# Kernel tuning notes

Measured on AMD Instinct MI355X. Metric: run time of the kernel, lower is better.

## Reference

```python
import jax, jax.numpy as jnp
import numpy as np

MAX_LENGTH = 64
SOS_TOKEN = 0
B, S, H, V = 32, 64, 512, 32000


def setup_inputs() -> dict:
    key = jax.random.key(0)
    ks = jax.random.split(key, 12)
    w = 0.02  # weight init scale to keep tanh/sigmoid in sane range
    return {
        "encoder_outputs": jax.random.normal(ks[0], (B, S, H), jnp.float32),
        "encoder_hidden": jax.random.normal(ks[1], (1, B, H), jnp.float32),
        "target_tensor": jax.random.randint(ks[2], (B, MAX_LENGTH), 0, V),
        "emb": jax.random.normal(ks[3], (V, H), jnp.float32) * w,
        "Wa": jax.random.normal(ks[4], (H, H), jnp.float32) * w,
        "ba": jnp.zeros((H,), jnp.float32),
        "Ua": jax.random.normal(ks[5], (H, H), jnp.float32) * w,
        "bu": jnp.zeros((H,), jnp.float32),
        "Va": jax.random.normal(ks[6], (1, H), jnp.float32) * w,
        "bv": jnp.zeros((1,), jnp.float32),
        "W_ih": jax.random.normal(ks[7], (3 * H, 2 * H), jnp.float32) * w,
        "b_ih": jnp.zeros((3 * H,), jnp.float32),
        "W_hh": jax.random.normal(ks[8], (3 * H, H), jnp.float32) * w,
        "b_hh": jnp.zeros((3 * H,), jnp.float32),
        "Wout": jax.random.normal(ks[9], (V, H), jnp.float32) * w,
        "bout": jnp.zeros((V,), jnp.float32),
    }


def reference(encoder_outputs, encoder_hidden, target_tensor, emb, Wa, ba, Ua, bu,
              Va, bv, W_ih, b_ih, W_hh, b_hh, Wout, bout):
    # Teacher-forced decode: step 0 uses SOS, step i uses target[:, i-1].
    tokens = jnp.concatenate(
        [jnp.full((target_tensor.shape[0], 1), SOS_TOKEN, target_tensor.dtype),
         target_tensor[:, :-1]], axis=1)  # [B, T]
    keys_proj = jnp.einsum('bsh,gh->bsg', encoder_outputs, Ua) + bu  # Ua(keys), step-invariant
    h_dim = encoder_hidden.shape[-1]
    va = Va[0]

    def step(h, tok):  # h: [B,H], tok: [B]
        x = emb[tok]                                   # embedding (dropout = identity in eval)
        q = h @ Wa.T + ba                              # Wa(query)  [B,H]
        e = jnp.tanh(q[:, None, :] + keys_proj)        # [B,S,H]
        scores = jnp.einsum('bsh,h->bs', e, va) + bv[0]
        w = jax.nn.softmax(scores, axis=-1)            # [B,S]
        context = jnp.einsum('bs,bsh->bh', w, encoder_outputs)
        xin = jnp.concatenate([x, context], axis=-1)   # [B,2H]
        gi = xin @ W_ih.T + b_ih                       # [B,3H]
        gh = h @ W_hh.T + b_hh
        r = jax.nn.sigmoid(gi[:, :h_dim] + gh[:, :h_dim])
        z = jax.nn.sigmoid(gi[:, h_dim:2 * h_dim] + gh[:, h_dim:2 * h_dim])
        n = jnp.tanh(gi[:, 2 * h_dim:] + r * gh[:, 2 * h_dim:])
        h_new = (1.0 - z) * n + z * h
        logits = h_new @ Wout.T + bout                 # [B,V]
        return h_new, (logits, w)

    h0 = encoder_hidden[0]
    hT, (logits, attn) = jax.lax.scan(step, h0, tokens.T)  # logits [T,B,V], attn [T,B,S]
    decoder_outputs = jax.nn.log_softmax(jnp.transpose(logits, (1, 0, 2)), axis=-1)
    attentions = jnp.transpose(attn, (1, 0, 2))
    return decoder_outputs, hT[None], attentions


if __name__ == "__main__":
    out = reference(**setup_inputs())
    print([o.shape for o in out])
```

## Files before the change

### kernel.cpp

```cpp
#include <hip/hip_runtime.h>
#include <stdint.h>

typedef __bf16 bf16;
typedef __bf16 bf16x4 __attribute__((ext_vector_type(4)));
typedef __bf16 bf16x8 __attribute__((ext_vector_type(8)));
typedef float f32x4 __attribute__((ext_vector_type(4)));

#define NB_REC 256

__device__ __forceinline__ float fast_tanh(float x) {
  x = fminf(fmaxf(x, -15.f), 15.f);
  float u = __expf(2.f * x);
  return (u - 1.f) / (u + 1.f);
}
__device__ __forceinline__ float fast_sigmoid(float x) {
  return 1.f / (1.f + __expf(-x));
}

__global__ __launch_bounds__(256) void f2bf_k(const float* __restrict__ s,
                                              bf16* __restrict__ d, long n) {
  long i = ((long)blockIdx.x * 256 + threadIdx.x) * 4;
  if (i >= n) return;
  float4 v = *(const float4*)(s + i);
  bf16x4 o = {(bf16)v.x, (bf16)v.y, (bf16)v.z, (bf16)v.w};
  *(bf16x4*)(d + i) = o;
}

__global__ __launch_bounds__(256) void split_wih_k(const float* __restrict__ W,
                                                   bf16* __restrict__ X,
                                                   bf16* __restrict__ Cc) {
  long i = ((long)blockIdx.x * 256 + threadIdx.x) * 4;
  if (i >= (long)1536 * 512) return;
  long j = i >> 9, k = i & 511;
  float4 a = *(const float4*)(W + j * 1024 + k);
  float4 b = *(const float4*)(W + j * 1024 + 512 + k);
  bf16x4 oa = {(bf16)a.x, (bf16)a.y, (bf16)a.z, (bf16)a.w};
  bf16x4 ob = {(bf16)b.x, (bf16)b.y, (bf16)b.z, (bf16)b.w};
  *(bf16x4*)(X + i) = oa;
  *(bf16x4*)(Cc + i) = ob;
}

__global__ __launch_bounds__(256) void embed_k(const int* __restrict__ tgt,
                                               const float* __restrict__ emb,
                                               bf16* __restrict__ xe) {
  long i = ((long)blockIdx.x * 256 + threadIdx.x) * 4;
  if (i >= (long)2048 * 512) return;
  long m = i >> 9, k = i & 511;
  int b = (int)(m >> 6), t = (int)(m & 63);
  int tok = (t == 0) ? 0 : tgt[b * 64 + t - 1];
  float4 v = *(const float4*)(emb + (long)tok * 512 + k);
  bf16x4 o = {(bf16)v.x, (bf16)v.y, (bf16)v.z, (bf16)v.w};
  *(bf16x4*)(xe + i) = o;
}

__global__ __launch_bounds__(256) void kpt_k(const float* __restrict__ kp,
                                             float* __restrict__ kpT) {
  long i = (long)blockIdx.x * 256 + threadIdx.x;
  if (i >= (long)32 * 512 * 64) return;
  int b = (int)(i >> 15);
  int r = (int)(i & 32767);
  int k = r >> 6, s = r & 63;
  kpT[i] = kp[((long)b * 64 + s) * 512 + k];
}

__global__ __launch_bounds__(256) void gemm_bt(const bf16* __restrict__ A,
                                               const bf16* __restrict__ Bm,
                                               const float* __restrict__ bias,
                                               float* __restrict__ C, int N) {
  __shared__ bf16 As[128 * 32];
  __shared__ bf16 Bs[128 * 32];
  const int tid = threadIdx.x;
  const int bx = blockIdx.x;
  const int bm = bx & 15;
  const int bn = bx >> 4;
  const int lane = tid & 63;
  const int w = tid >> 6;
  const int l16 = lane & 15, q4 = lane >> 4;
  const int wm = (w & 1) * 64, wn = (w >> 1) * 64;
  const long m0 = (long)bm * 128;
  const long n0 = (long)bn * 128;
  const int r0 = tid >> 2;
  const int kp8 = (tid & 3) * 8;

  f32x4 acc[4][4] = {};
  for (int kk = 0; kk < 512; kk += 32) {
    __syncthreads();
    {
      bf16x8 va0 = *(const bf16x8*)(A + (m0 + r0) * 512 + kk + kp8);
      bf16x8 va1 = *(const bf16x8*)(A + (m0 + 64 + r0) * 512 + kk + kp8);
      bf16x8 vb0 = *(const bf16x8*)(Bm + (n0 + r0) * 512 + kk + kp8);
      bf16x8 vb1 = *(const bf16x8*)(Bm + (n0 + 64 + r0) * 512 + kk + kp8);
      *(bf16x8*)&As[r0 * 32 + kp8] = va0;
      *(bf16x8*)&As[(64 + r0) * 32 + kp8] = va1;
      *(bf16x8*)&Bs[r0 * 32 + kp8] = vb0;
      *(bf16x8*)&Bs[(64 + r0) * 32 + kp8] = vb1;
    }
    __syncthreads();
    bf16x8 af[4], bfr[4];
#pragma unroll
    for (int i = 0; i < 4; ++i)
      af[i] = *(const bf16x8*)&As[(wm + i * 16 + l16) * 32 + q4 * 8];
#pragma unroll
    for (int j = 0; j < 4; ++j)
      bfr[j] = *(const bf16x8*)&Bs[(wn + j * 16 + l16) * 32 + q4 * 8];
#pragma unroll
    for (int i = 0; i < 4; ++i)
#pragma unroll
      for (int j = 0; j < 4; ++j)
        acc[i][j] = __builtin_amdgcn_mfma_f32_16x16x32_bf16(af[i], bfr[j], acc[i][j], 0, 0, 0);
  }
#pragma unroll
  for (int i = 0; i < 4; ++i) {
    const long rbase = m0 + wm + i * 16 + q4 * 4;
#pragma unroll
    for (int j = 0; j < 4; ++j) {
      const long col = n0 + wn + j * 16 + l16;
      const float bv = bias ? bias[col] : 0.f;
      f32x4 a = acc[i][j];
      C[(rbase + 0) * N + col] = a[0] + bv;
      C[(rbase + 1) * N + col] = a[1] + bv;
      C[(rbase + 2) * N + col] = a[2] + bv;
      C[(rbase + 3) * N + col] = a[3] + bv;
    }
  }
}

__device__ __forceinline__ void gbar(unsigned* bar, int g, unsigned epoch) {
  __syncthreads();
  if (threadIdx.x == 0) {
    __builtin_amdgcn_s_waitcnt(0);
    __atomic_signal_fence(__ATOMIC_SEQ_CST);
    unsigned a = __hip_atomic_fetch_add(&bar[(g >> 5) * 16], 1u,
                                        __ATOMIC_RELAXED, __HIP_MEMORY_SCOPE_AGENT);
    if ((a & 31u) == 31u)
      __hip_atomic_fetch_add(&bar[128], 1u, __ATOMIC_RELAXED, __HIP_MEMORY_SCOPE_AGENT);
    while (__hip_atomic_load(&bar[128], __ATOMIC_RELAXED, __HIP_MEMORY_SCOPE_AGENT) <
           epoch * 8u)
      __builtin_amdgcn_s_sleep(2);
    __atomic_signal_fence(__ATOMIC_SEQ_CST);
  }
  __syncthreads();
}

__device__ __forceinline__ unsigned long long coh_load_u64(const unsigned long long* p) {
  return __hip_atomic_load(p, __ATOMIC_RELAXED, __HIP_MEMORY_SCOPE_AGENT);
}
__device__ __forceinline__ float coh_load_f32(const float* p) {
  return __hip_atomic_load(p, __ATOMIC_RELAXED, __HIP_MEMORY_SCOPE_AGENT);
}

__global__ __launch_bounds__(256) void recurrence_k(
    const bf16* __restrict__ Wc,
    const float* __restrict__ ba,
    const float* __restrict__ bhh,
    const float* __restrict__ ehid,
    unsigned long long* __restrict__ h_bfg,
    bf16* __restrict__ histb,
    float* __restrict__ QG,
    const float* __restrict__ kpT,
    const float* __restrict__ va,
    const float* __restrict__ gix,
    const float* __restrict__ ep,
    float* __restrict__ outhT,
    float* __restrict__ outattn,
    unsigned* __restrict__ bar) {
  const int g = blockIdx.x;
  const int tid = threadIdx.x;
  const int b = g & 31;
  const int p = g >> 5;
  __shared__ float va_s[512], q_s[512], part_s[256], w_s[64];
  __shared__ float gi_s[192], gh_s[192], h_loc[64];
  unsigned epoch = 0;

  va_s[tid] = va[tid];
  va_s[256 + tid] = va[256 + tid];
  if (tid < 64) h_loc[tid] = ehid[b * 512 + p * 64 + tid];
  if (g < 32 && tid < 128) {
    const float* hr = ehid + g * 512 + tid * 4;
    union { bf16 h[4]; unsigned long long u; } cv;
    cv.h[0] = (bf16)hr[0]; cv.h[1] = (bf16)hr[1];
    cv.h[2] = (bf16)hr[2]; cv.h[3] = (bf16)hr[3];
    __hip_atomic_store(&h_bfg[g * 128 + tid], cv.u, __ATOMIC_RELAXED,
                       __HIP_MEMORY_SCOPE_AGENT);
  }
  ++epoch;
  gbar(bar, g, epoch);

  for (int t = 0; t < 64; ++t) {
    if (g < 128 && tid < 64) {
      const int l16 = tid & 15, q4 = tid >> 4;
      const int n0 = g * 16;
      const bf16* bp = Wc + (long)(n0 + l16) * 512 + q4 * 8;
      const unsigned long long* a0p = h_bfg + l16 * 128 + q4 * 2;
      const unsigned long long* a1p = h_bfg + (16 + l16) * 128 + q4 * 2;
      f32x4 acc0 = {}, acc1 = {};
#pragma unroll
      for (int it = 0; it < 16; ++it) {
        union { unsigned long long u[2]; bf16x8 v; } A0, A1;
        A0.u[0] = coh_load_u64(a0p + it * 8 + 0);
        A0.u[1] = coh_load_u64(a0p + it * 8 + 1);
        A1.u[0] = coh_load_u64(a1p + it * 8 + 0);
        A1.u[1] = coh_load_u64(a1p + it * 8 + 1);
        bf16x8 bb = *(const bf16x8*)(bp + it * 32);
        acc0 = __builtin_amdgcn_mfma_f32_16x16x32_bf16(A0.v, bb, acc0, 0, 0, 0);
        acc1 = __builtin_amdgcn_mfma_f32_16x16x32_bf16(A1.v, bb, acc1, 0, 0, 0);
      }
      const int col = n0 + l16;
      const float badd = (col < 512) ? ba[col] : bhh[col - 512];
#pragma unroll
      for (int r = 0; r < 4; ++r) {
        __hip_atomic_store(&QG[(q4 * 4 + r) * 2048 + col], acc0[r] + badd,
                           __ATOMIC_RELAXED, __HIP_MEMORY_SCOPE_AGENT);
        __hip_atomic_store(&QG[(16 + q4 * 4 + r) * 2048 + col], acc1[r] + badd,
                           __ATOMIC_RELAXED, __HIP_MEMORY_SCOPE_AGENT);
      }
    }
    ++epoch;
    gbar(bar, g, epoch);

    q_s[tid] = coh_load_f32(&QG[b * 2048 + tid]);
    q_s[256 + tid] = coh_load_f32(&QG[b * 2048 + 256 + tid]);
    if (tid < 192) {
      const int part = tid >> 6, jj = tid & 63;
      gh_s[tid] = coh_load_f32(&QG[b * 2048 + 512 + part * 512 + p * 64 + jj]);
    }
    __syncthreads();

    {
      const int w = tid >> 6, l = tid & 63;
      const float* kprow = kpT + ((long)b * 512 + w * 128) * 64 + l;
      float acc = 0.f;
#pragma unroll 4
      for (int k = 0; k < 128; ++k)
        acc += va_s[w * 128 + k] * fast_tanh(q_s[w * 128 + k] + kprow[(long)k * 64]);
      part_s[w * 64 + l] = acc;
    }
    __syncthreads();
    if (tid < 64) {
      float sc = part_s[tid] + part_s[64 + tid] + part_s[128 + tid] + part_s[192 + tid];
      float e = __expf(sc);
      float sum = e;
#pragma unroll
      for (int d = 1; d < 64; d <<= 1) sum += __shfl_xor(sum, d);
      float wv = e / sum;
      w_s[tid] = wv;
      if (p == 0) outattn[(long)(b * 64 + t) * 64 + tid] = wv;
    }
    __syncthreads();

    if (tid < 192) {
      const int part = tid >> 6, jj = tid & 63;
      const int col = part * 512 + p * 64 + jj;
      const float* er = ep + (long)(b * 64) * 1536 + col;
      float acc = 0.f;
#pragma unroll 8
      for (int s2 = 0; s2 < 64; ++s2) acc += w_s[s2] * er[(long)s2 * 1536];
      gi_s[tid] = acc + gix[(long)(b * 64 + t) * 1536 + col];
    }
    __syncthreads();

    if (tid < 64) {
      float rr = fast_sigmoid(gi_s[tid] + gh_s[tid]);
      float zz = fast_sigmoid(gi_s[64 + tid] + gh_s[64 + tid]);
      float nn = fast_tanh(gi_s[128 + tid] + rr * gh_s[128 + tid]);
      float hp = h_loc[tid];
      float hn = (1.f - zz) * nn + zz * hp;
      h_loc[tid] = hn;
      const int j = p * 64 + tid;
      histb[(long)(b * 64 + t) * 512 + j] = (bf16)hn;
      if (t == 63) outhT[b * 512 + j] = hn;
      float hn1 = __shfl_xor(hn, 1);
      if ((tid & 1) == 0) {
        union { bf16 h[2]; unsigned u; } cv;
        cv.h[0] = (bf16)hn; cv.h[1] = (bf16)hn1;
        unsigned* h32v = (unsigned*)h_bfg;
        __hip_atomic_store(&h32v[b * 256 + (j >> 1)], cv.u, __ATOMIC_RELAXED,
                           __HIP_MEMORY_SCOPE_AGENT);
      }
    }
    ++epoch;
    gbar(bar, g, epoch);
  }
}

__global__ __launch_bounds__(256) void logsm_k(float* __restrict__ C) {
  const long row = blockIdx.x;
  float* x = C + row * 32000L;
  const int tid = threadIdx.x;
  __shared__ float red[4];
  float s = 0.f;
  for (long i = (long)tid * 4; i < 32000; i += 1024) {
    float4 v = *(const float4*)(x + i);
    s += __expf(v.x);
    s += __expf(v.y);
    s += __expf(v.z);
    s += __expf(v.w);
  }
#pragma unroll
  for (int d = 1; d < 64; d <<= 1) s += __shfl_xor(s, d);
  if ((tid & 63) == 0) red[tid >> 6] = s;
  __syncthreads();
  const float lse = __logf(red[0] + red[1] + red[2] + red[3]);
  for (long i = (long)tid * 4; i < 32000; i += 1024) {
    float4 v = *(const float4*)(x + i);
    v.x -= lse; v.y -= lse; v.z -= lse; v.w -= lse;
    *(float4*)(x + i) = v;
  }
}

extern "C" void kernel_launch(void* const* d_in, const int* in_sizes, int n_in,
                              void* d_out, int out_size, void* d_ws, size_t ws_size,
                              hipStream_t stream) {
  const float* enc  = (const float*)d_in[0];
  const float* ehid = (const float*)d_in[1];
  const int* tgt    = (const int*)d_in[2];
  const float* emb  = (const float*)d_in[3];
  const float* Wa   = (const float*)d_in[4];
  const float* ba   = (const float*)d_in[5];
  const float* Ua   = (const float*)d_in[6];
  const float* bu   = (const float*)d_in[7];
  const float* Va   = (const float*)d_in[8];
  const float* Wih  = (const float*)d_in[10];
  const float* bih  = (const float*)d_in[11];
  const float* Whh  = (const float*)d_in[12];
  const float* bhh  = (const float*)d_in[13];
  const float* Wout = (const float*)d_in[14];
  const float* bout = (const float*)d_in[15];

  char* ws = (char*)d_ws;
  size_t off = 0;
  auto alloc = [&](size_t bytes) {
    void* pp = ws + off;
    off += (bytes + 255) & ~(size_t)255;
    return pp;
  };
  unsigned* bar  = (unsigned*)alloc(1024);
  unsigned long long* h_bfg = (unsigned long long*)alloc((long)32 * 128 * 8);
  bf16* enc_bf   = (bf16*)alloc((long)2048 * 512 * 2);
  bf16* Wc_bf    = (bf16*)alloc((long)2048 * 512 * 2);
  bf16* Ua_bf    = (bf16*)alloc((long)512 * 512 * 2);
  bf16* Wihx_bf  = (bf16*)alloc((long)1536 * 512 * 2);
  bf16* Wihc_bf  = (bf16*)alloc((long)1536 * 512 * 2);
  bf16* xemb_bf  = (bf16*)alloc((long)2048 * 512 * 2);
  bf16* histb    = (bf16*)alloc((long)2048 * 512 * 2);
  bf16* Wout_bf  = (bf16*)alloc((long)32000 * 512 * 2);
  float* kp      = (float*)alloc((long)2048 * 512 * 4);
  float* kpT     = (float*)alloc((long)32 * 512 * 64 * 4);
  float* gix     = (float*)alloc((long)2048 * 1536 * 4);
  float* ep      = (float*)alloc((long)2048 * 1536 * 4);
  float* QG      = (float*)alloc((long)32 * 2048 * 4);
  (void)ws_size; (void)in_sizes; (void)n_in; (void)out_size;

  float* out0   = (float*)d_out;
  float* outhT  = out0 + (long)2048 * 32000;
  float* outatt = outhT + (long)32 * 512;

  hipMemsetAsync(bar, 0, 1024, stream);

  dim3 blk(256);
  f2bf_k<<<dim3(1024), blk, 0, stream>>>(enc, enc_bf, (long)2048 * 512);
  f2bf_k<<<dim3(256), blk, 0, stream>>>(Ua, Ua_bf, (long)512 * 512);
  f2bf_k<<<dim3(16000), blk, 0, stream>>>(Wout, Wout_bf, (long)32000 * 512);
  f2bf_k<<<dim3(256), blk, 0, stream>>>(Wa, Wc_bf, (long)512 * 512);
  f2bf_k<<<dim3(768), blk, 0, stream>>>(Whh, Wc_bf + (long)512 * 512, (long)1536 * 512);
  split_wih_k<<<dim3(768), blk, 0, stream>>>(Wih, Wihx_bf, Wihc_bf);
  embed_k<<<dim3(1024), blk, 0, stream>>>(tgt, emb, xemb_bf);

  gemm_bt<<<dim3(16 * 4), blk, 0, stream>>>(enc_bf, Ua_bf, bu, kp, 512);
  kpt_k<<<dim3(4096), blk, 0, stream>>>(kp, kpT);
  gemm_bt<<<dim3(16 * 12), blk, 0, stream>>>(xemb_bf, Wihx_bf, bih, gix, 1536);
  gemm_bt<<<dim3(16 * 12), blk, 0, stream>>>(enc_bf, Wihc_bf, (const float*)nullptr, ep, 1536);

  recurrence_k<<<dim3(NB_REC), blk, 0, stream>>>(Wc_bf, ba, bhh, ehid, h_bfg, histb,
                                                 QG, kpT, Va, gix, ep, outhT, outatt, bar);

  gemm_bt<<<dim3(16 * 250), blk, 0, stream>>>(histb, Wout_bf, bout, out0, 32000);
  logsm_k<<<dim3(2048), blk, 0, stream>>>(out0);
}
```

Baseline: 2.023 ms.

## Replace centralized hidden-state GEMM with per-block partial products, one barrier per step

Previously each step used two grid-wide barriers: one after 128 blocks computed the [32x2048] Wa/Whh projection with MFMA from a shared bf16 hidden state, and one after the hidden update. Now each block multiplies its own 64-element slice of h against the matching Wc columns, writes 8-way partial sums into a double-buffered scratch array, and consumers sum the 8 partials plus biases. This removes one grid barrier per timestep. In exchange, every block does scalar FMA work over 2048 outputs and reads 8x more data from global memory when reducing the partials.

```diff
diff --git a/kernel.cpp b/kernel.cpp
--- a/kernel.cpp
+++ b/kernel.cpp
@@ -142,11 +142,37 @@
   __syncthreads();
 }
 
-__device__ __forceinline__ unsigned long long coh_load_u64(const unsigned long long* p) {
-  return __hip_atomic_load(p, __ATOMIC_RELAXED, __HIP_MEMORY_SCOPE_AGENT);
-}
 __device__ __forceinline__ float coh_load_f32(const float* p) {
   return __hip_atomic_load(p, __ATOMIC_RELAXED, __HIP_MEMORY_SCOPE_AGENT);
+}
+__device__ __forceinline__ void coh_store_f32(float* p, float v) {
+  __hip_atomic_store(p, v, __ATOMIC_RELAXED, __HIP_MEMORY_SCOPE_AGENT);
+}
+
+__device__ __forceinline__ void publish_partials(const bf16* __restrict__ Wc,
+                                                 const float* h_bf,
+                                                 float* __restrict__ dst,
+                                                 int tid, int p) {
+  float hv[64];
+#pragma unroll
+  for (int k = 0; k < 16; ++k) {
+    f32x4 h4 = *(const f32x4*)(h_bf + k * 4);
+    hv[k * 4 + 0] = h4[0]; hv[k * 4 + 1] = h4[1];
+    hv[k * 4 + 2] = h4[2]; hv[k * 4 + 3] = h4[3];
+  }
+  const bf16* wbase = Wc + (long)tid * 512 + p * 64;
+#pragma unroll
+  for (int r = 0; r < 8; ++r) {
+    const bf16* wr = wbase + (long)r * (256 * 512);
+    float acc = 0.f;
+#pragma unroll
+    for (int i = 0; i < 8; ++i) {
+      bf16x8 wv = *(const bf16x8*)(wr + i * 8);
+#pragma unroll
+      for (int u = 0; u < 8; ++u) acc = fmaf(hv[i * 8 + u], (float)wv[u], acc);
+    }
+    coh_store_f32(dst + tid + 256 * r, acc);
+  }
 }
 
 __global__ __launch_bounds__(256) void recurrence_k(
@@ -154,9 +180,8 @@
     const float* __restrict__ ba,
     const float* __restrict__ bhh,
     const float* __restrict__ ehid,
-    unsigned long long* __restrict__ h_bfg,
     bf16* __restrict__ histb,
-    float* __restrict__ QG,
+    float* __restrict__ qp,
     const float* __restrict__ kpT,
     const float* __restrict__ va,
     const float* __restrict__ gix,
@@ -168,72 +193,61 @@
   const int tid = threadIdx.x;
   const int b = g & 31;
   const int p = g >> 5;
-  __shared__ float va_s[512], q_s[512], part_s[256], w_s[64];
+  __shared__ float va_s[512], ba_s[512], bhh_s[192];
+  __shared__ float q_s[512], part_s[256], w_s[64];
   __shared__ float gi_s[192], gh_s[192], h_loc[64];
+  __shared__ __align__(16) float h_bf[64];
   unsigned epoch = 0;
 
-  va_s[tid] = va[tid];
-  va_s[256 + tid] = va[256 + tid];
-  if (tid < 64) h_loc[tid] = ehid[b * 512 + p * 64 + tid];
-  if (g < 32 && tid < 128) {
-    const float* hr = ehid + g * 512 + tid * 4;
-    union { bf16 h[4]; unsigned long long u; } cv;
-    cv.h[0] = (bf16)hr[0]; cv.h[1] = (bf16)hr[1];
-    cv.h[2] = (bf16)hr[2]; cv.h[3] = (bf16)hr[3];
-    __hip_atomic_store(&h_bfg[g * 128 + tid], cv.u, __ATOMIC_RELAXED,
-                       __HIP_MEMORY_SCOPE_AGENT);
-  }
+  va_s[tid] = va[tid];       va_s[256 + tid] = va[256 + tid];
+  ba_s[tid] = ba[tid];       ba_s[256 + tid] = ba[256 + tid];
+  if (tid < 192) {
+    const int part = tid >> 6, jj = tid & 63;
+    bhh_s[tid] = bhh[part * 512 + p * 64 + jj];
+  }
+  if (tid < 64) {
+    float hp = ehid[b * 512 + p * 64 + tid];
+    h_loc[tid] = hp;
+    h_bf[tid] = (float)(bf16)hp;
+  }
+  __syncthreads();
+
+  publish_partials(Wc, h_bf, qp + ((long)b * 8 + p) * 2048, tid, p);
   ++epoch;
   gbar(bar, g, epoch);
 
+  const int wv_ = tid >> 6, ln = tid & 63;
+
   for (int t = 0; t < 64; ++t) {
-    if (g < 128 && tid < 64) {
-      const int l16 = tid & 15, q4 = tid >> 4;
-      const int n0 = g * 16;
-      const bf16* bp = Wc + (long)(n0 + l16) * 512 + q4 * 8;
-      const unsigned long long* a0p = h_bfg + l16 * 128 + q4 * 2;
-      const unsigned long long* a1p = h_bfg + (16 + l16) * 128 + q4 * 2;
-      f32x4 acc0 = {}, acc1 = {};
-#pragma unroll
-      for (int it = 0; it < 16; ++it) {
-        union { unsigned long long u[2]; bf16x8 v; } A0, A1;
-        A0.u[0] = coh_load_u64(a0p + it * 8 + 0);
-        A0.u[1] = coh_load_u64(a0p + it * 8 + 1);
-        A1.u[0] = coh_load_u64(a1p + it * 8 + 0);
-        A1.u[1] = coh_load_u64(a1p + it * 8 + 1);
-        bf16x8 bb = *(const bf16x8*)(bp + it * 32);
-        acc0 = __builtin_amdgcn_mfma_f32_16x16x32_bf16(A0.v, bb, acc0, 0, 0, 0);
-        acc1 = __builtin_amdgcn_mfma_f32_16x16x32_bf16(A1.v, bb, acc1, 0, 0, 0);
+    const int par = t & 1;
+    const float* src = qp + (((long)par * 32 + b) * 8) * 2048;
+
+    {
+      const int k0 = wv_ * 128 + ln;
+      float q0 = ba_s[k0], q1 = ba_s[k0 + 64];
+#pragma unroll
+      for (int pp = 0; pp < 8; ++pp) {
+        q0 += coh_load_f32(src + pp * 2048 + k0);
+        q1 += coh_load_f32(src + pp * 2048 + k0 + 64);
       }
-      const int col = n0 + l16;
-      const float badd = (col < 512) ? ba[col] : bhh[col - 512];
-#pragma unroll
-      for (int r = 0; r < 4; ++r) {
-        __hip_atomic_store(&QG[(q4 * 4 + r) * 2048 + col], acc0[r] + badd,
-                           __ATOMIC_RELAXED, __HIP_MEMORY_SCOPE_AGENT);
-        __hip_atomic_store(&QG[(16 + q4 * 4 + r) * 2048 + col], acc1[r] + badd,
-                           __ATOMIC_RELAXED, __HIP_MEMORY_SCOPE_AGENT);
-      }
-    }
-    ++epoch;
-    gbar(bar, g, epoch);
-
-    q_s[tid] = coh_load_f32(&QG[b * 2048 + tid]);
-    q_s[256 + tid] = coh_load_f32(&QG[b * 2048 + 256 + tid]);
+      q_s[k0] = q0;
+      q_s[k0 + 64] = q1;
+    }
     if (tid < 192) {
-      const int part = tid >> 6, jj = tid & 63;
-      gh_s[tid] = coh_load_f32(&QG[b * 2048 + 512 + part * 512 + p * 64 + jj]);
-    }
-    __syncthreads();
+      const int n = 512 + (tid >> 6) * 512 + p * 64 + (tid & 63);
+      float gg = bhh_s[tid];
+#pragma unroll
+      for (int pp = 0; pp < 8; ++pp) gg += coh_load_f32(src + pp * 2048 + n);
+      gh_s[tid] = gg;
+    }
 
     {
-      const int w = tid >> 6, l = tid & 63;
-      const float* kprow = kpT + ((long)b * 512 + w * 128) * 64 + l;
+      const float* kprow = kpT + ((long)b * 512 + wv_ * 128) * 64 + ln;
       float acc = 0.f;
 #pragma unroll 4
       for (int k = 0; k < 128; ++k)
-        acc += va_s[w * 128 + k] * fast_tanh(q_s[w * 128 + k] + kprow[(long)k * 64]);
-      part_s[w * 64 + l] = acc;
+        acc += va_s[wv_ * 128 + k] * fast_tanh(q_s[wv_ * 128 + k] + kprow[(long)k * 64]);
+      part_s[tid] = acc;
     }
     __syncthreads();
     if (tid < 64) {
@@ -242,9 +256,9 @@
       float sum = e;
 #pragma unroll
       for (int d = 1; d < 64; d <<= 1) sum += __shfl_xor(sum, d);
-      float wv = e / sum;
-      w_s[tid] = wv;
-      if (p == 0) outattn[(long)(b * 64 + t) * 64 + tid] = wv;
+      float wvx = e / sum;
+      w_s[tid] = wvx;
+      if (p == 0) outattn[(long)(b * 64 + t) * 64 + tid] = wvx;
     }
     __syncthreads();
 
@@ -266,20 +280,20 @@
       float hp = h_loc[tid];
       float hn = (1.f - zz) * nn + zz * hp;
       h_loc[tid] = hn;
+      bf16 hb = (bf16)hn;
+      h_bf[tid] = (float)hb;
       const int j = p * 64 + tid;
-      histb[(long)(b * 64 + t) * 512 + j] = (bf16)hn;
+      histb[(long)(b * 64 + t) * 512 + j] = hb;
       if (t == 63) outhT[b * 512 + j] = hn;
-      float hn1 = __shfl_xor(hn, 1);
-      if ((tid & 1) == 0) {
-        union { bf16 h[2]; unsigned u; } cv;
-        cv.h[0] = (bf16)hn; cv.h[1] = (bf16)hn1;
-        unsigned* h32v = (unsigned*)h_bfg;
-        __hip_atomic_store(&h32v[b * 256 + (j >> 1)], cv.u, __ATOMIC_RELAXED,
-                           __HIP_MEMORY_SCOPE_AGENT);
-      }
-    }
-    ++epoch;
-    gbar(bar, g, epoch);
+    }
+    __syncthreads();
+
+    if (t < 63) {
+      publish_partials(Wc, h_bf,
+                       qp + (((long)(par ^ 1) * 32 + b) * 8 + p) * 2048, tid, p);
+      ++epoch;
+      gbar(bar, g, epoch);
+    }
   }
 }
 
@@ -335,7 +349,7 @@
     return pp;
   };
   unsigned* bar  = (unsigned*)alloc(1024);
-  unsigned long long* h_bfg = (unsigned long long*)alloc((long)32 * 128 * 8);
+  float* qp      = (float*)alloc((long)2 * 32 * 8 * 2048 * 4);
   bf16* enc_bf   = (bf16*)alloc((long)2048 * 512 * 2);
   bf16* Wc_bf    = (bf16*)alloc((long)2048 * 512 * 2);
   bf16* Ua_bf    = (bf16*)alloc((long)512 * 512 * 2);
@@ -348,7 +362,6 @@
   float* kpT     = (float*)alloc((long)32 * 512 * 64 * 4);
   float* gix     = (float*)alloc((long)2048 * 1536 * 4);
   float* ep      = (float*)alloc((long)2048 * 1536 * 4);
-  float* QG      = (float*)alloc((long)32 * 2048 * 4);
   (void)ws_size; (void)in_sizes; (void)n_in; (void)out_size;
 
   float* out0   = (float*)d_out;
@@ -371,8 +384,8 @@
   gemm_bt<<<dim3(16 * 12), blk, 0, stream>>>(xemb_bf, Wihx_bf, bih, gix, 1536);
   gemm_bt<<<dim3(16 * 12), blk, 0, stream>>>(enc_bf, Wihc_bf, (const float*)nullptr, ep, 1536);
 
-  recurrence_k<<<dim3(NB_REC), blk, 0, stream>>>(Wc_bf, ba, bhh, ehid, h_bfg, histb,
-                                                 QG, kpT, Va, gix, ep, outhT, outatt, bar);
+  recurrence_k<<<dim3(NB_REC), blk, 0, stream>>>(Wc_bf, ba, bhh, ehid, histb, qp,
+                                                 kpT, Va, gix, ep, outhT, outatt, bar);
 
   gemm_bt<<<dim3(16 * 250), blk, 0, stream>>>(histb, Wout_bf, bout, out0, 32000);
   logsm_k<<<dim3(2048), blk, 0, stream>>>(out0);
```

New measurement: 4.146 ms. +105.0%, slower.

## Cache keys projection in LDS and split recurrent MFMA K-loop across waves

Applied to the files above, without the earlier changes.

Each persistent block loads its batch row's 128KB projected-keys slab into shared memory once, so the per-step attention tanh loop no longer re-reads it from global memory. The recurrent hidden GEMV K-loop is now spread over all four waves instead of one, with partial accumulators summed through LDS before wave 0 stores. The gix load for the step is also issued early so its latency overlaps the GEMV. In exchange the kernel uses about 128KB of LDS per block, which limits it to one block per CU, and each step gains an extra __syncthreads.

```diff
diff --git a/kernel.cpp b/kernel.cpp
--- a/kernel.cpp
+++ b/kernel.cpp
@@ -168,13 +168,20 @@
   const int tid = threadIdx.x;
   const int b = g & 31;
   const int p = g >> 5;
+  __shared__ float kp_s[512 * 64];
   __shared__ float va_s[512], q_s[512], part_s[256], w_s[64];
   __shared__ float gi_s[192], gh_s[192], h_loc[64];
+  __shared__ f32x4 red_p1[3][2][64];
   unsigned epoch = 0;
 
   va_s[tid] = va[tid];
   va_s[256 + tid] = va[256 + tid];
   if (tid < 64) h_loc[tid] = ehid[b * 512 + p * 64 + tid];
+  {
+    const float* kpb = kpT + (long)b * 512 * 64;
+    for (int i = tid * 4; i < 512 * 64; i += 1024)
+      *(f32x4*)&kp_s[i] = *(const f32x4*)(kpb + i);
+  }
   if (g < 32 && tid < 128) {
     const float* hr = ehid + g * 512 + tid * 4;
     union { bf16 h[4]; unsigned long long u; } cv;
@@ -186,16 +193,30 @@
   ++epoch;
   gbar(bar, g, epoch);
 
+  const int wv_ = tid >> 6, ln = tid & 63;
+  const int l16 = ln & 15, q4 = ln >> 4;
+  const bf16* bp = nullptr;
+  const unsigned long long *a0p = nullptr, *a1p = nullptr;
+  float badd = 0.f;
+  if (g < 128) {
+    const int n0 = g * 16;
+    bp  = Wc + (long)(n0 + l16) * 512 + q4 * 8;
+    a0p = h_bfg + l16 * 128 + q4 * 2;
+    a1p = h_bfg + (16 + l16) * 128 + q4 * 2;
+    const int col = n0 + l16;
+    badd = (col < 512) ? ba[col] : bhh[col - 512];
+  }
+
   for (int t = 0; t < 64; ++t) {
-    if (g < 128 && tid < 64) {
-      const int l16 = tid & 15, q4 = tid >> 4;
-      const int n0 = g * 16;
-      const bf16* bp = Wc + (long)(n0 + l16) * 512 + q4 * 8;
-      const unsigned long long* a0p = h_bfg + l16 * 128 + q4 * 2;
-      const unsigned long long* a1p = h_bfg + (16 + l16) * 128 + q4 * 2;
+    float gval = 0.f;
+    if (tid < 192)
+      gval = gix[(long)(b * 64 + t) * 1536 + (tid >> 6) * 512 + p * 64 + (tid & 63)];
+
+    if (g < 128) {
       f32x4 acc0 = {}, acc1 = {};
 #pragma unroll
-      for (int it = 0; it < 16; ++it) {
+      for (int it2 = 0; it2 < 4; ++it2) {
+        const int it = wv_ * 4 + it2;
         union { unsigned long long u[2]; bf16x8 v; } A0, A1;
         A0.u[0] = coh_load_u64(a0p + it * 8 + 0);
         A0.u[1] = coh_load_u64(a0p + it * 8 + 1);
@@ -205,14 +226,22 @@
         acc0 = __builtin_amdgcn_mfma_f32_16x16x32_bf16(A0.v, bb, acc0, 0, 0, 0);
         acc1 = __builtin_amdgcn_mfma_f32_16x16x32_bf16(A1.v, bb, acc1, 0, 0, 0);
       }
-      const int col = n0 + l16;
-      const float badd = (col < 512) ? ba[col] : bhh[col - 512];
-#pragma unroll
-      for (int r = 0; r < 4; ++r) {
-        __hip_atomic_store(&QG[(q4 * 4 + r) * 2048 + col], acc0[r] + badd,
-                           __ATOMIC_RELAXED, __HIP_MEMORY_SCOPE_AGENT);
-        __hip_atomic_store(&QG[(16 + q4 * 4 + r) * 2048 + col], acc1[r] + badd,
-                           __ATOMIC_RELAXED, __HIP_MEMORY_SCOPE_AGENT);
+      if (wv_) { red_p1[wv_ - 1][0][ln] = acc0; red_p1[wv_ - 1][1][ln] = acc1; }
+      __syncthreads();
+      if (wv_ == 0) {
+#pragma unroll
+        for (int r = 0; r < 3; ++r) {
+          acc0 += red_p1[r][0][ln];
+          acc1 += red_p1[r][1][ln];
+        }
+        const int col = g * 16 + l16;
+#pragma unroll
+        for (int r = 0; r < 4; ++r) {
+          __hip_atomic_store(&QG[(q4 * 4 + r) * 2048 + col], acc0[r] + badd,
+                             __ATOMIC_RELAXED, __HIP_MEMORY_SCOPE_AGENT);
+          __hip_atomic_store(&QG[(16 + q4 * 4 + r) * 2048 + col], acc1[r] + badd,
+                             __ATOMIC_RELAXED, __HIP_MEMORY_SCOPE_AGENT);
+        }
       }
     }
     ++epoch;
@@ -227,13 +256,12 @@
     __syncthreads();
 
     {
-      const int w = tid >> 6, l = tid & 63;
-      const float* kprow = kpT + ((long)b * 512 + w * 128) * 64 + l;
+      const float* kprow = &kp_s[(wv_ * 128) * 64 + ln];
       float acc = 0.f;
-#pragma unroll 4
+#pragma unroll 8
       for (int k = 0; k < 128; ++k)
-        acc += va_s[w * 128 + k] * fast_tanh(q_s[w * 128 + k] + kprow[(long)k * 64]);
-      part_s[w * 64 + l] = acc;
+        acc += va_s[wv_ * 128 + k] * fast_tanh(q_s[wv_ * 128 + k] + kprow[k * 64]);
+      part_s[wv_ * 64 + ln] = acc;
     }
     __syncthreads();
     if (tid < 64) {
@@ -242,9 +270,9 @@
       float sum = e;
 #pragma unroll
       for (int d = 1; d < 64; d <<= 1) sum += __shfl_xor(sum, d);
-      float wv = e / sum;
-      w_s[tid] = wv;
-      if (p == 0) outattn[(long)(b * 64 + t) * 64 + tid] = wv;
+      float wvx = e / sum;
+      w_s[tid] = wvx;
+      if (p == 0) outattn[(long)(b * 64 + t) * 64 + tid] = wvx;
     }
     __syncthreads();
 
@@ -255,7 +283,7 @@
       float acc = 0.f;
 #pragma unroll 8
       for (int s2 = 0; s2 < 64; ++s2) acc += w_s[s2] * er[(long)s2 * 1536];
-      gi_s[tid] = acc + gix[(long)(b * 64 + t) * 1536 + col];
+      gi_s[tid] = acc + gval;
     }
     __syncthreads();
 
```

New measurement: 1.718 ms. -15.0%, faster.
